# Kernel tuning notes

Hardware: AMD Instinct MI355X
Metric: run time of the kernel (lower is better)

Reference implementation:

```python
import jax, jax.numpy as jnp
import numpy as np

ALPHA = 0.2  # LeakyReLU negative slope
NEG_INF = -9e15


def setup_inputs() -> dict:
    key = jax.random.key(0)
    ks = jax.random.split(key, 6)
    B, N, F_in, F_out = 16, 1024, 1024, 512
    x = jax.random.normal(ks[0], (B, N, F_in), dtype=jnp.float32)
    adj = jax.random.randint(ks[1], (B, N, N), 0, 2, dtype=jnp.int32)
    W = jax.random.normal(ks[2], (F_in, F_out), dtype=jnp.float32) * 0.02
    a = jax.random.normal(ks[3], (2 * F_out, 1), dtype=jnp.float32) * 0.02
    fc_w = jax.random.normal(ks[4], (F_out, 2 * F_out), dtype=jnp.float32) * 0.02
    fc_b = jnp.zeros((F_out,), dtype=jnp.float32)
    return {"x": x, "adj": adj, "W": W, "a": a, "fc_w": fc_w, "fc_b": fc_b}


def reference(x, adj, W, a, fc_w, fc_b):
    # h: [B, N, F_out]
    h = jnp.matmul(x, W)
    F_out = W.shape[1]
    # The original builds a_input = concat(h_i, h_j) of shape [B,N,N,2F] and
    # contracts with a. Equivalently (same math, no O(N^2 F) intermediate):
    # e_ij = leakyrelu(h_i . a[:F] + h_j . a[F:])
    a1 = a[:F_out, 0]  # [F_out]
    a2 = a[F_out:, 0]  # [F_out]
    f1 = jnp.einsum('bnf,f->bn', h, a1)  # source term
    f2 = jnp.einsum('bnf,f->bn', h, a2)  # target term
    e = jax.nn.leaky_relu(f1[:, :, None] + f2[:, None, :], negative_slope=ALPHA)  # [B,N,N]
    attention = jnp.where(adj > 0, e, jnp.full_like(e, NEG_INF))
    attention = jax.nn.softmax(attention, axis=2)
    # dropout is identity in eval mode
    agg = jnp.matmul(attention, h)  # [B,N,F_out]
    h_prime = jnp.concatenate([agg, h], axis=2)  # [B,N,2F]
    h_prime = jnp.matmul(h_prime, fc_w.T) + fc_b
    return jax.nn.elu(h_prime)  # concat=True path
```

## Files before the change

kernel.cpp:

```cpp
#include <hip/hip_runtime.h>

#define ALPHA 0.2f

typedef __attribute__((ext_vector_type(8))) short short8;
typedef __attribute__((ext_vector_type(4))) float f32x4;

__device__ __forceinline__ unsigned short f2b(float f) {
  unsigned int u; __builtin_memcpy(&u, &f, 4);
  unsigned int r = (u + 0x7FFFu + ((u >> 16) & 1u)) >> 16;
  return (unsigned short)r;
}
__device__ __forceinline__ float b2f(unsigned short v) {
  unsigned int u = ((unsigned int)v) << 16; float f; __builtin_memcpy(&f, &u, 4); return f;
}
__device__ __forceinline__ void gl_lds16(const unsigned short* g, unsigned short* l) {
  __builtin_amdgcn_global_load_lds((__attribute__((address_space(1))) void*)g,
                                   (__attribute__((address_space(3))) void*)l, 16, 0, 0);
}

__device__ __forceinline__ void cvt_f4(const float* __restrict__ in,
                                       unsigned short* __restrict__ out,
                                       unsigned int f4idx) {
  float4 v = ((const float4*)in)[f4idx];
  alignas(8) unsigned short o[4];
  o[0] = f2b(v.x); o[1] = f2b(v.y); o[2] = f2b(v.z); o[3] = f2b(v.w);
  ((uint2*)out)[f4idx] = *(const uint2*)o;
}

__global__ __launch_bounds__(256) void prep1(const int* __restrict__ adj,
                                             unsigned short* __restrict__ bm16,
                                             const float* __restrict__ x,
                                             unsigned short* __restrict__ xb,
                                             const float* __restrict__ fcw,
                                             unsigned short* __restrict__ fcwb,
                                             const float* __restrict__ W,
                                             unsigned short* __restrict__ Wt) {
  __shared__ alignas(16) unsigned short tile[64][72];
  unsigned int bx = blockIdx.x;
  unsigned int tid = threadIdx.x;
  if (bx < 4096u) {
    unsigned int gw = bx * 4u + (tid >> 6);
    int lane = tid & 63;
    const int4* a4 = (const int4*)adj + (size_t)gw * 256;
    unsigned short* ob = bm16 + (size_t)gw * 64;
    #pragma unroll
    for (int t = 0; t < 4; t++) {
      int4 v = a4[t * 64 + lane];
      unsigned nib = (unsigned)(v.x > 0) | ((unsigned)(v.y > 0) << 1) |
                     ((unsigned)(v.z > 0) << 2) | ((unsigned)(v.w > 0) << 3);
      unsigned n1 = __shfl_down(nib, 1);
      unsigned n2 = __shfl_down(nib, 2);
      unsigned n3 = __shfl_down(nib, 3);
      if ((lane & 3) == 0)
        ob[t * 16 + (lane >> 2)] =
            (unsigned short)(nib | (n1 << 4) | (n2 << 8) | (n3 << 12));
    }
  } else if (bx < 12288u) {
    unsigned int base = (bx - 4096u) * 512u;
    cvt_f4(x, xb, base + tid);
    cvt_f4(x, xb, base + 256u + tid);
  } else if (bx < 12544u) {
    unsigned int base = (bx - 12288u) * 512u;
    cvt_f4(fcw, fcwb, base + tid);
    cvt_f4(fcw, fcwb, base + 256u + tid);
  } else {
    unsigned int idx = bx - 12544u;
    unsigned int k0 = (idx >> 3) * 64, n0 = (idx & 7) * 64;
    #pragma unroll
    for (int p = 0; p < 4; p++) {
      int r = p * 16 + (tid >> 4);
      int c = (tid & 15) * 4;
      float4 v = *(const float4*)(W + (size_t)(k0 + r) * 512 + n0 + c);
      tile[r][c] = f2b(v.x); tile[r][c + 1] = f2b(v.y);
      tile[r][c + 2] = f2b(v.z); tile[r][c + 3] = f2b(v.w);
    }
    __syncthreads();
    int f = tid >> 2;
    int ic = (tid & 3) * 16;
    alignas(16) unsigned short buf[16];
    #pragma unroll
    for (int k = 0; k < 16; k++) buf[k] = tile[ic + k][f];
    uint4* dst = (uint4*)(Wt + (size_t)(n0 + f) * 1024 + k0 + ic);
    dst[0] = ((const uint4*)buf)[0];
    dst[1] = ((const uint4*)buf)[1];
  }
}

__global__ __launch_bounds__(256) void prep2(const unsigned short* __restrict__ hp,
                                             const float* __restrict__ a,
                                             float* __restrict__ f1, float* __restrict__ f2,
                                             unsigned short* __restrict__ ht) {
  __shared__ alignas(16) unsigned short tile[64][72];
  int bx = blockIdx.x;
  int tid = threadIdx.x;
  if (bx < 4096) {
    int row = bx * 4 + (tid >> 6);
    int lane = tid & 63;
    const unsigned short* hrow = hp + (size_t)row * 1024 + 512;
    uint4 raw = *(const uint4*)(hrow + lane * 8);
    alignas(16) unsigned short hv[8]; __builtin_memcpy(hv, &raw, 16);
    float s1 = 0.f, s2 = 0.f;
    #pragma unroll
    for (int j = 0; j < 8; j++) {
      float hf = b2f(hv[j]);
      s1 += hf * a[lane * 8 + j];
      s2 += hf * a[512 + lane * 8 + j];
    }
    #pragma unroll
    for (int o = 32; o > 0; o >>= 1) { s1 += __shfl_down(s1, o); s2 += __shfl_down(s2, o); }
    if (lane == 0) { f1[row] = s1; f2[row] = s2; }
  } else {
    int idx = bx - 4096;
    int b = idx >> 7;
    int f0 = ((idx >> 4) & 7) * 64;
    int i0 = (idx & 15) * 64;
    #pragma unroll
    for (int p = 0; p < 2; p++) {
      int r = p * 32 + (tid >> 3);
      int c = (tid & 7) * 8;
      uint4 v = *(const uint4*)(hp + (size_t)(b * 1024 + i0 + r) * 1024 + 512 + f0 + c);
      *(uint4*)(&tile[r][c]) = v;
    }
    __syncthreads();
    int f = tid >> 2;
    int ic = (tid & 3) * 16;
    alignas(16) unsigned short buf[16];
    #pragma unroll
    for (int k = 0; k < 16; k++) buf[k] = tile[ic + k][f];
    uint4* dst = (uint4*)(ht + (size_t)(b * 512 + f0 + f) * 1024 + i0 + ic);
    dst[0] = ((const uint4*)buf)[0];
    dst[1] = ((const uint4*)buf)[1];
  }
}

__global__ __launch_bounds__(256) void rowsum_P(const unsigned short* __restrict__ bm16,
                                                const float* __restrict__ f1,
                                                const float* __restrict__ f2,
                                                float* __restrict__ invl,
                                                unsigned short* __restrict__ P) {
  int row = blockIdx.x * 4 + (threadIdx.x >> 6);
  int lane = threadIdx.x & 63;
  int b = row >> 10;
  float f1v = f1[row];
  unsigned int bits = bm16[(size_t)row * 64 + lane];
  const float* f2p = f2 + (b << 10) + lane * 16;
  float4 v0 = ((const float4*)f2p)[0];
  float4 v1 = ((const float4*)f2p)[1];
  float4 v2 = ((const float4*)f2p)[2];
  float4 v3 = ((const float4*)f2p)[3];
  float fv[16] = {v0.x, v0.y, v0.z, v0.w, v1.x, v1.y, v1.z, v1.w,
                  v2.x, v2.y, v2.z, v2.w, v3.x, v3.y, v3.z, v3.w};
  float s = 0.f;
  alignas(16) unsigned short o[16];
  #pragma unroll
  for (int j = 0; j < 16; j++) {
    float p = 0.f;
    if ((bits >> j) & 1u) {
      float z = f1v + fv[j];
      z = z > 0.f ? z : ALPHA * z;
      p = __expf(z);
      s += p;
    }
    o[j] = f2b(p);
  }
  uint4* dst = (uint4*)(P + (size_t)row * 1024 + lane * 16);
  dst[0] = ((const uint4*)o)[0];
  dst[1] = ((const uint4*)o)[1];
  #pragma unroll
  for (int off = 32; off > 0; off >>= 1) s += __shfl_down(s, off);
  if (lane == 0) invl[row] = 1.0f / s;
}

template <int EPI>
__global__ __launch_bounds__(256) void gemm_bt(
    const unsigned short* __restrict__ A, size_t aBS,
    const unsigned short* __restrict__ Bt, size_t bBS,
    int K,
    void* __restrict__ outp, size_t oBS, int ldo, int ocol,
    const float* __restrict__ scale,
    const float* __restrict__ bias) {
  __shared__ alignas(16) unsigned short As[2 * 128 * 64];
  __shared__ alignas(16) unsigned short Bs[2 * 128 * 64];
  const int tid = threadIdx.x;
  const int lane = tid & 63;
  const int w = tid >> 6;
  const int m0 = blockIdx.x * 128;
  const int n0 = blockIdx.y * 128;
  const int zb = blockIdx.z;
  const unsigned short* Ab = A + (size_t)zb * aBS;
  const unsigned short* Btb = Bt + (size_t)zb * bBS;

  f32x4 acc[4][4];
  #pragma unroll
  for (int i = 0; i < 4; i++)
    #pragma unroll
    for (int j = 0; j < 4; j++)
      #pragma unroll
      for (int r = 0; r < 4; r++) acc[i][j][r] = 0.f;

  const int lr = lane >> 3;
  const int lc = (lane & 7) ^ (lr & 7);
  const unsigned short* ag = Ab + (size_t)(m0 + w * 32 + lr) * K + lc * 8;
  const unsigned short* bg = Btb + (size_t)(n0 + w * 32 + lr) * K + lc * 8;
  const int sbase = w * 32 * 64;

  const int wm = (w & 1) * 64;
  const int wn = (w >> 1) * 64;
  const int row16 = lane & 15;
  const int quad = lane >> 4;
  const int sw = row16 & 7;

  #pragma unroll
  for (int t = 0; t < 4; t++) {
    gl_lds16(ag + (size_t)(t * 8) * K, As + sbase + t * 512);
    gl_lds16(bg + (size_t)(t * 8) * K, Bs + sbase + t * 512);
  }
  __syncthreads();

  int bufo = 0;
  for (int k0 = 0; k0 < K; k0 += 64) {
    const int nbufo = bufo ^ 8192;
    if (k0 + 64 < K) {
      #pragma unroll
      for (int t = 0; t < 4; t++) {
        gl_lds16(ag + (k0 + 64) + (size_t)(t * 8) * K, As + nbufo + sbase + t * 512);
        gl_lds16(bg + (k0 + 64) + (size_t)(t * 8) * K, Bs + nbufo + sbase + t * 512);
      }
    }
    short8 af[2][4], bf[2][4];
    #pragma unroll
    for (int s = 0; s < 2; s++) {
      #pragma unroll
      for (int i = 0; i < 4; i++) {
        af[s][i] = *(const short8*)(As + bufo + (wm + i * 16 + row16) * 64 + ((s * 4 + quad) ^ sw) * 8);
        bf[s][i] = *(const short8*)(Bs + bufo + (wn + i * 16 + row16) * 64 + ((s * 4 + quad) ^ sw) * 8);
      }
    }
    #pragma unroll
    for (int s = 0; s < 2; s++)
      #pragma unroll
      for (int am = 0; am < 4; am++)
        #pragma unroll
        for (int bn = 0; bn < 4; bn++)
          acc[am][bn] = __builtin_amdgcn_mfma_f32_16x16x32_bf16(af[s][am], bf[s][bn], acc[am][bn], 0, 0, 0);
    __syncthreads();
    bufo = nbufo;
  }

  const int col = lane & 15;
  const int r0 = quad * 4;
  #pragma unroll
  for (int am = 0; am < 4; am++) {
    #pragma unroll
    for (int bn = 0; bn < 4; bn++) {
      #pragma unroll
      for (int r = 0; r < 4; r++) {
        int m = m0 + wm + am * 16 + r0 + r;
        int n = n0 + wn + bn * 16 + col;
        float v = acc[am][bn][r];
        if (EPI == 3) v *= scale[zb * 1024 + m];
        if (EPI == 2) {
          v += bias[n];
          v = v > 0.f ? v : expm1f(v);
          ((float*)outp)[(size_t)m * ldo + n] = v;
        } else {
          ((unsigned short*)outp)[(size_t)zb * oBS + (size_t)m * ldo + ocol + n] = f2b(v);
        }
      }
    }
  }
}

extern "C" void kernel_launch(void* const* d_in, const int* in_sizes, int n_in,
                              void* d_out, int out_size, void* d_ws, size_t ws_size,
                              hipStream_t stream) {
  const float* x   = (const float*)d_in[0];
  const int*   adj = (const int*)d_in[1];
  const float* W   = (const float*)d_in[2];
  const float* a   = (const float*)d_in[3];
  const float* fcw = (const float*)d_in[4];
  const float* fcb = (const float*)d_in[5];
  float* out = (float*)d_out;
  char* ws = (char*)d_ws;

  unsigned short* xb   = (unsigned short*)(ws);
  unsigned short* hp   = (unsigned short*)(ws + 33554432);
  unsigned short* ht   = (unsigned short*)(ws + 67108864);
  unsigned short* Wt   = (unsigned short*)(ws + 83886080);
  unsigned short* fcwb = (unsigned short*)(ws + 84934656);
  float* f1            = (float*)(ws + 85983232);
  float* f2            = (float*)(ws + 86048768);
  float* invl          = (float*)(ws + 86114304);
  unsigned short* bm   = (unsigned short*)(ws + 86179840);
  unsigned short* P = xb;

  prep1<<<12672, 256, 0, stream>>>(adj, bm, x, xb, fcw, fcwb, W, Wt);

  gemm_bt<1><<<dim3(128, 4, 1), 256, 0, stream>>>(xb, 0, Wt, 0, 1024,
                                                  hp, 0, 1024, 512, nullptr, nullptr);
  prep2<<<6144, 256, 0, stream>>>(hp, a, f1, f2, ht);
  rowsum_P<<<4096, 256, 0, stream>>>(bm, f1, f2, invl, P);

  gemm_bt<3><<<dim3(8, 4, 16), 256, 0, stream>>>(P, 1024 * 1024, ht, 512 * 1024, 1024,
                                                 hp, 1024 * 1024, 1024, 0, invl, nullptr);
  gemm_bt<2><<<dim3(128, 4, 1), 256, 0, stream>>>(hp, 0, fcwb, 0, 1024,
                                                  out, 0, 512, 0, nullptr, fcb);
}
```

Before: 265.7 us.

## Fuse fp32-to-bf16 conversion of x into GEMM and read adj directly in rowsum

Result: faster. 260.2 us (-2.1%).

```diff
diff --git a/kernel.cpp b/kernel.cpp
--- a/kernel.cpp
+++ b/kernel.cpp
@@ -16,6 +16,12 @@
 __device__ __forceinline__ void gl_lds16(const unsigned short* g, unsigned short* l) {
   __builtin_amdgcn_global_load_lds((__attribute__((address_space(1))) void*)g,
                                    (__attribute__((address_space(3))) void*)l, 16, 0, 0);
+}
+__device__ __forceinline__ uint4 pack8(float4 v0, float4 v1) {
+  alignas(16) unsigned short o[8];
+  o[0] = f2b(v0.x); o[1] = f2b(v0.y); o[2] = f2b(v0.z); o[3] = f2b(v0.w);
+  o[4] = f2b(v1.x); o[5] = f2b(v1.y); o[6] = f2b(v1.z); o[7] = f2b(v1.w);
+  return *(const uint4*)o;
 }
 
 __device__ __forceinline__ void cvt_f4(const float* __restrict__ in,
@@ -27,44 +33,19 @@
   ((uint2*)out)[f4idx] = *(const uint2*)o;
 }
 
-__global__ __launch_bounds__(256) void prep1(const int* __restrict__ adj,
-                                             unsigned short* __restrict__ bm16,
-                                             const float* __restrict__ x,
-                                             unsigned short* __restrict__ xb,
-                                             const float* __restrict__ fcw,
+__global__ __launch_bounds__(256) void prep1(const float* __restrict__ fcw,
                                              unsigned short* __restrict__ fcwb,
                                              const float* __restrict__ W,
                                              unsigned short* __restrict__ Wt) {
   __shared__ alignas(16) unsigned short tile[64][72];
   unsigned int bx = blockIdx.x;
   unsigned int tid = threadIdx.x;
-  if (bx < 4096u) {
-    unsigned int gw = bx * 4u + (tid >> 6);
-    int lane = tid & 63;
-    const int4* a4 = (const int4*)adj + (size_t)gw * 256;
-    unsigned short* ob = bm16 + (size_t)gw * 64;
-    #pragma unroll
-    for (int t = 0; t < 4; t++) {
-      int4 v = a4[t * 64 + lane];
-      unsigned nib = (unsigned)(v.x > 0) | ((unsigned)(v.y > 0) << 1) |
-                     ((unsigned)(v.z > 0) << 2) | ((unsigned)(v.w > 0) << 3);
-      unsigned n1 = __shfl_down(nib, 1);
-      unsigned n2 = __shfl_down(nib, 2);
-      unsigned n3 = __shfl_down(nib, 3);
-      if ((lane & 3) == 0)
-        ob[t * 16 + (lane >> 2)] =
-            (unsigned short)(nib | (n1 << 4) | (n2 << 8) | (n3 << 12));
-    }
-  } else if (bx < 12288u) {
-    unsigned int base = (bx - 4096u) * 512u;
-    cvt_f4(x, xb, base + tid);
-    cvt_f4(x, xb, base + 256u + tid);
-  } else if (bx < 12544u) {
-    unsigned int base = (bx - 12288u) * 512u;
+  if (bx < 256u) {
+    unsigned int base = bx * 512u;
     cvt_f4(fcw, fcwb, base + tid);
     cvt_f4(fcw, fcwb, base + 256u + tid);
   } else {
-    unsigned int idx = bx - 12544u;
+    unsigned int idx = bx - 256u;
     unsigned int k0 = (idx >> 3) * 64, n0 = (idx & 7) * 64;
     #pragma unroll
     for (int p = 0; p < 4; p++) {
@@ -133,7 +114,7 @@
   }
 }
 
-__global__ __launch_bounds__(256) void rowsum_P(const unsigned short* __restrict__ bm16,
+__global__ __launch_bounds__(256) void rowsum_P(const int* __restrict__ adj,
                                                 const float* __restrict__ f1,
                                                 const float* __restrict__ f2,
                                                 float* __restrict__ invl,
@@ -142,7 +123,13 @@
   int lane = threadIdx.x & 63;
   int b = row >> 10;
   float f1v = f1[row];
-  unsigned int bits = bm16[(size_t)row * 64 + lane];
+  const int4* ap = (const int4*)(adj + (size_t)row * 1024) + lane * 4;
+  int4 a0 = ap[0];
+  int4 a1 = ap[1];
+  int4 a2 = ap[2];
+  int4 a3 = ap[3];
+  int av[16] = {a0.x, a0.y, a0.z, a0.w, a1.x, a1.y, a1.z, a1.w,
+                a2.x, a2.y, a2.z, a2.w, a3.x, a3.y, a3.z, a3.w};
   const float* f2p = f2 + (b << 10) + lane * 16;
   float4 v0 = ((const float4*)f2p)[0];
   float4 v1 = ((const float4*)f2p)[1];
@@ -155,7 +142,7 @@
   #pragma unroll
   for (int j = 0; j < 16; j++) {
     float p = 0.f;
-    if ((bits >> j) & 1u) {
+    if (av[j] > 0) {
       float z = f1v + fv[j];
       z = z > 0.f ? z : ALPHA * z;
       p = __expf(z);
@@ -171,9 +158,9 @@
   if (lane == 0) invl[row] = 1.0f / s;
 }
 
-template <int EPI>
+template <int EPI, int CVTA>
 __global__ __launch_bounds__(256) void gemm_bt(
-    const unsigned short* __restrict__ A, size_t aBS,
+    const void* __restrict__ A_, size_t aBS,
     const unsigned short* __restrict__ Bt, size_t bBS,
     int K,
     void* __restrict__ outp, size_t oBS, int ldo, int ocol,
@@ -187,7 +174,6 @@
   const int m0 = blockIdx.x * 128;
   const int n0 = blockIdx.y * 128;
   const int zb = blockIdx.z;
-  const unsigned short* Ab = A + (size_t)zb * aBS;
   const unsigned short* Btb = Bt + (size_t)zb * bBS;
 
   f32x4 acc[4][4];
@@ -200,9 +186,15 @@
 
   const int lr = lane >> 3;
   const int lc = (lane & 7) ^ (lr & 7);
-  const unsigned short* ag = Ab + (size_t)(m0 + w * 32 + lr) * K + lc * 8;
+  const unsigned short* ag = nullptr;
+  const float* agf = nullptr;
+  if (CVTA)
+    agf = (const float*)A_ + (size_t)zb * aBS + (size_t)(m0 + w * 32 + lr) * K + lc * 8;
+  else
+    ag = (const unsigned short*)A_ + (size_t)zb * aBS + (size_t)(m0 + w * 32 + lr) * K + lc * 8;
   const unsigned short* bg = Btb + (size_t)(n0 + w * 32 + lr) * K + lc * 8;
   const int sbase = w * 32 * 64;
+  const int lofs = lane * 8;
 
   const int wm = (w & 1) * 64;
   const int wn = (w >> 1) * 64;
@@ -210,22 +202,48 @@
   const int quad = lane >> 4;
   const int sw = row16 & 7;
 
-  #pragma unroll
-  for (int t = 0; t < 4; t++) {
-    gl_lds16(ag + (size_t)(t * 8) * K, As + sbase + t * 512);
-    gl_lds16(bg + (size_t)(t * 8) * K, Bs + sbase + t * 512);
+  if (CVTA) {
+    float4 av[4][2];
+    #pragma unroll
+    for (int t = 0; t < 4; t++) {
+      av[t][0] = *(const float4*)(agf + (size_t)(t * 8) * K);
+      av[t][1] = *(const float4*)(agf + (size_t)(t * 8) * K + 4);
+    }
+    #pragma unroll
+    for (int t = 0; t < 4; t++)
+      gl_lds16(bg + (size_t)(t * 8) * K, Bs + sbase + t * 512);
+    #pragma unroll
+    for (int t = 0; t < 4; t++)
+      *(uint4*)(As + sbase + t * 512 + lofs) = pack8(av[t][0], av[t][1]);
+  } else {
+    #pragma unroll
+    for (int t = 0; t < 4; t++) {
+      gl_lds16(ag + (size_t)(t * 8) * K, As + sbase + t * 512);
+      gl_lds16(bg + (size_t)(t * 8) * K, Bs + sbase + t * 512);
+    }
   }
   __syncthreads();
 
   int bufo = 0;
   for (int k0 = 0; k0 < K; k0 += 64) {
     const int nbufo = bufo ^ 8192;
-    if (k0 + 64 < K) {
-      #pragma unroll
-      for (int t = 0; t < 4; t++) {
-        gl_lds16(ag + (k0 + 64) + (size_t)(t * 8) * K, As + nbufo + sbase + t * 512);
+    const bool pf = (k0 + 64 < K);
+    float4 av[4][2];
+    if (pf) {
+      if (CVTA) {
+        #pragma unroll
+        for (int t = 0; t < 4; t++) {
+          av[t][0] = *(const float4*)(agf + (k0 + 64) + (size_t)(t * 8) * K);
+          av[t][1] = *(const float4*)(agf + (k0 + 64) + (size_t)(t * 8) * K + 4);
+        }
+      } else {
+        #pragma unroll
+        for (int t = 0; t < 4; t++)
+          gl_lds16(ag + (k0 + 64) + (size_t)(t * 8) * K, As + nbufo + sbase + t * 512);
+      }
+      #pragma unroll
+      for (int t = 0; t < 4; t++)
         gl_lds16(bg + (k0 + 64) + (size_t)(t * 8) * K, Bs + nbufo + sbase + t * 512);
-      }
     }
     short8 af[2][4], bf[2][4];
     #pragma unroll
@@ -243,6 +261,11 @@
         #pragma unroll
         for (int bn = 0; bn < 4; bn++)
           acc[am][bn] = __builtin_amdgcn_mfma_f32_16x16x32_bf16(af[s][am], bf[s][bn], acc[am][bn], 0, 0, 0);
+    if (pf && CVTA) {
+      #pragma unroll
+      for (int t = 0; t < 4; t++)
+        *(uint4*)(As + nbufo + sbase + t * 512 + lofs) = pack8(av[t][0], av[t][1]);
+    }
     __syncthreads();
     bufo = nbufo;
   }
@@ -283,7 +306,7 @@
   float* out = (float*)d_out;
   char* ws = (char*)d_ws;
 
-  unsigned short* xb   = (unsigned short*)(ws);
+  unsigned short* P    = (unsigned short*)(ws);
   unsigned short* hp   = (unsigned short*)(ws + 33554432);
   unsigned short* ht   = (unsigned short*)(ws + 67108864);
   unsigned short* Wt   = (unsigned short*)(ws + 83886080);
@@ -291,18 +314,16 @@
   float* f1            = (float*)(ws + 85983232);
   float* f2            = (float*)(ws + 86048768);
   float* invl          = (float*)(ws + 86114304);
-  unsigned short* bm   = (unsigned short*)(ws + 86179840);
-  unsigned short* P = xb;
-
-  prep1<<<12672, 256, 0, stream>>>(adj, bm, x, xb, fcw, fcwb, W, Wt);
-
-  gemm_bt<1><<<dim3(128, 4, 1), 256, 0, stream>>>(xb, 0, Wt, 0, 1024,
-                                                  hp, 0, 1024, 512, nullptr, nullptr);
+
+  prep1<<<384, 256, 0, stream>>>(fcw, fcwb, W, Wt);
+
+  gemm_bt<1, 1><<<dim3(128, 4, 1), 256, 0, stream>>>(x, 0, Wt, 0, 1024,
+                                                     hp, 0, 1024, 512, nullptr, nullptr);
   prep2<<<6144, 256, 0, stream>>>(hp, a, f1, f2, ht);
-  rowsum_P<<<4096, 256, 0, stream>>>(bm, f1, f2, invl, P);
-
-  gemm_bt<3><<<dim3(8, 4, 16), 256, 0, stream>>>(P, 1024 * 1024, ht, 512 * 1024, 1024,
-                                                 hp, 1024 * 1024, 1024, 0, invl, nullptr);
-  gemm_bt<2><<<dim3(128, 4, 1), 256, 0, stream>>>(hp, 0, fcwb, 0, 1024,
-                                                  out, 0, 512, 0, nullptr, fcb);
-}
+  rowsum_P<<<4096, 256, 0, stream>>>(adj, f1, f2, invl, P);
+
+  gemm_bt<3, 0><<<dim3(8, 4, 16), 256, 0, stream>>>(P, 1024 * 1024, ht, 512 * 1024, 1024,
+                                                    hp, 1024 * 1024, 1024, 0, invl, nullptr);
+  gemm_bt<2, 0><<<dim3(128, 4, 1), 256, 0, stream>>>(hp, 0, fcwb, 0, 1024,
+                                                     out, 0, 512, 0, nullptr, fcb);
+}
```
